# Kernel optimization log

Measured on AMD Instinct MI355X. Metric: run time of the kernel, lower is better.

The kernel has to match this reference:

```python
import jax, jax.numpy as jnp
import numpy as np

NINPUTS = 16
WIDTH = 128
KSIZE = 21
SPP = 8
BS, CI, H, W = 2, 3, 192, 192
EPS = 1e-08


def _conv(x, w, b, padding):
    y = jax.lax.conv_general_dilated(
        x, w, window_strides=(1, 1), padding=padding,
        dimension_numbers=("NCHW", "OIHW", "NCHW"))
    return y + b[None, :, None, None]


def apply_kernels(kernel, radiance, ksize):
    """Per-pixel predicted-kernel conv: fused gather-multiply-reduce over taps.
    kernel: (bs, ksize^2, kh, kw), radiance: (bs, ci, h, w).
    Replicates torch apply_kernels (normalization='sum') without materializing
    the (bs, ci, kh, kw, ksize^2) unfold tile tensor."""
    bs, k2, kh, kw = kernel.shape
    _, ci, h, w = radiance.shape
    needed = kh + ksize - 1
    if needed > h:
        crop = (needed - h) // 2
        if crop > 0:
            kernel = kernel[:, :, crop:-crop, crop:-crop]
        kh, kw = kernel.shape[2], kernel.shape[3]
    else:
        crop = (h - needed) // 2
        if crop > 0:
            radiance = radiance[:, :, crop:-crop, crop:-crop]
    taps = jnp.arange(k2, dtype=jnp.int32)
    dy = taps // ksize
    dx = taps % ksize

    def body(acc, idx):
        patch = jax.lax.dynamic_slice(radiance, (0, 0, dy[idx], dx[idx]),
                                      (bs, ci, kh, kw))
        kv = jax.lax.dynamic_slice_in_dim(kernel, idx, 1, axis=1)  # (bs,1,kh,kw)
        return acc + kv * patch, None

    acc0 = jnp.zeros((bs, ci, kh, kw), radiance.dtype)
    weighted_sum, _ = jax.lax.scan(body, acc0, taps)
    kernel_sum = jnp.sum(kernel, axis=1, keepdims=True)  # (bs,1,kh,kw)
    return weighted_sum, kernel_sum


def setup_inputs() -> dict:
    key = jax.random.key(0)
    ks = jax.random.split(key, 10)
    s = 0.05
    inp = {
        "features": jax.random.normal(ks[0], (BS, SPP, NINPUTS, H, W), jnp.float32),
        "radiance": jax.random.uniform(ks[1], (BS, SPP, CI, H, W), jnp.float32),
        # recurrent conv processor (simplified main_processor): SAME 3x3 conv
        "w_rnn": jax.random.normal(ks[2], (WIDTH, NINPUTS + WIDTH, 3, 3), jnp.float32) * s,
        "b_rnn": jnp.zeros((WIDTH,), jnp.float32),
        "w_k1": jax.random.normal(ks[3], (WIDTH, WIDTH + NINPUTS, 3, 3), jnp.float32) * s,
        "b_k1": jnp.zeros((WIDTH,), jnp.float32),
        "w_k2": jax.random.normal(ks[4], (WIDTH, WIDTH, 3, 3), jnp.float32) * s,
        "b_k2": jnp.zeros((WIDTH,), jnp.float32),
        "w_k3": jax.random.normal(ks[5], (KSIZE * KSIZE, WIDTH, 3, 3), jnp.float32) * s,
        "b_k3": jnp.zeros((KSIZE * KSIZE,), jnp.float32),
    }
    return inp


def reference(features, radiance, w_rnn, b_rnn, w_k1, b_k1, w_k2, b_k2, w_k3, b_k3):
    bs, spp, ci, h, w = radiance.shape
    lrelu = lambda x: jax.nn.leaky_relu(x, 0.01)
    state = jnp.zeros((bs, WIDTH, h, w), features.dtype)
    unnorm = sumw = max_k = None
    for step in range(spp):
        f = features[:, step]  # (bs, ninputs, h, w)
        rnn = lrelu(_conv(jnp.concatenate([f, state], axis=1), w_rnn, b_rnn, "SAME"))
        state = rnn
        nf = jnp.concatenate([rnn, f], axis=1)  # (bs, width+ninputs, h, w)
        k = lrelu(_conv(nf, w_k1, b_k1, "VALID"))
        k = lrelu(_conv(k, w_k2, b_k2, "VALID"))
        k = _conv(k, w_k3, b_k3, "VALID")  # (bs, ksize^2, h-6, w-6), linear out
        # online-softmax (flash-attention-style) running max/exp rescale
        new_max = jnp.max(k.reshape(bs, -1), axis=1).reshape(bs, 1, 1, 1)
        if step == 0:
            max_k = new_max
        else:
            old_max = max_k
            max_k = jnp.maximum(old_max, new_max)
        kern = jnp.exp(k - max_k)
        ws, ksum = apply_kernels(kern, radiance[:, step], KSIZE)
        if step == 0:
            unnorm, sumw = ws, ksum
        else:
            scale = jnp.exp(old_max - max_k)
            unnorm = unnorm * scale + ws
            sumw = sumw * scale + ksum
    return unnorm / (sumw + EPS)
```

## Files before the change

kernel.cpp:

```cpp
#include <hip/hip_runtime.h>
#include <stdint.h>

typedef _Float16 half8 __attribute__((ext_vector_type(8)));
typedef _Float16 half4 __attribute__((ext_vector_type(4)));
typedef __attribute__((ext_vector_type(8))) short short8;
typedef __attribute__((ext_vector_type(4))) float f32x4;

__device__ __forceinline__ unsigned encf(float x){
  uint32_t u = __float_as_uint(x);
  return (u & 0x80000000u) ? ~u : (u | 0x80000000u);
}
__device__ __forceinline__ float decf(unsigned u){
  uint32_t b = (u & 0x80000000u) ? (u & 0x7FFFFFFFu) : ~u;
  return __uint_as_float(b);
}
__device__ __forceinline__ void gload16(const void* g, void* l){
  __builtin_amdgcn_global_load_lds(
      (const __attribute__((address_space(1))) void*)g,
      (__attribute__((address_space(3))) void*)l, 16, 0, 0);
}

__global__ __launch_bounds__(256) void zero_u32(unsigned* __restrict__ p, int n){
  for (int i = blockIdx.x*256 + threadIdx.x; i < n; i += gridDim.x*256) p[i] = 0u;
}

__global__ __launch_bounds__(256) void pack_w(const float* __restrict__ w, _Float16* __restrict__ wp,
                                              int CO, int CI, int COP, int CINP){
  int idx = blockIdx.x*256 + threadIdx.x;
  int total = 9*COP*CINP;
  if (idx >= total) return;
  int ci = idx % CINP;
  int rest = idx / CINP;
  int co = rest % COP;
  int t  = rest / COP;
  float v = 0.f;
  if (co < CO && ci < CI) v = w[((size_t)co*CI + ci)*9 + t];
  int kc = ci >> 5, cr = ci & 31;
  wp[(((size_t)kc*9 + t)*COP + co)*32 + cr] = (_Float16)v;
}

__global__ __launch_bounds__(256) void pack_bias(const float* __restrict__ b, float* __restrict__ bp, int n, int npad){
  int i = blockIdx.x*256 + threadIdx.x;
  if (i < npad) bp[i] = (i < n) ? b[i] : 0.f;
}

__global__ __launch_bounds__(256) void pack_feat(const float* __restrict__ f,
                                                 _Float16* __restrict__ rnn_in,
                                                 _Float16* __restrict__ k1_in,
                                                 int copy_state,
                                                 unsigned fbstr, unsigned rbstr, unsigned kbstr){
  int p = blockIdx.x*256 + threadIdx.x;
  if (p >= 36864) return;
  int b = blockIdx.y;
  int y = p / 192, x = p % 192;
  const float* fb = f + (size_t)b*fbstr;
  _Float16* r = rnn_in + (size_t)b*rbstr + ((size_t)(y+1)*194 + (x+1))*160;
  _Float16* k = k1_in  + (size_t)b*kbstr + (size_t)p*160;
  #pragma unroll
  for (int c = 0; c < 16; ++c){
    _Float16 v = (_Float16)fb[c*36864 + p];
    r[c] = v;
    k[128 + c] = v;
  }
  if (copy_state){
    #pragma unroll
    for (int cc = 0; cc < 128; cc += 8)
      *reinterpret_cast<short8*>(r + 16 + cc) = *reinterpret_cast<const short8*>(k + cc);
  }
}

template<int CINP, bool RELU, bool K3>
__global__ __launch_bounds__(256, 3) void conv3(
    const _Float16* __restrict__ X, int Wst, unsigned xbstr,
    const _Float16* __restrict__ Wp, int COP,
    const float* __restrict__ bias,
    _Float16* __restrict__ Y, int Wst_out, int DCP, unsigned ybstr,
    unsigned* __restrict__ slot, int Ho, int Wo,
    int nco_mask, int nco_shift)
{
  constexpr int KC = CINP/32;
  __shared__ _Float16 lds[2][6528];

  const int tid  = threadIdx.x;
  const int lane = tid & 63;
  const int wid  = tid >> 6;
  const int wm   = wid & 1;
  const int wq   = wid >> 1;
  const int l15  = lane & 15, lg = lane >> 4;
  const int xb   = blockIdx.x * 32;
  const int yb   = blockIdx.y * 4;
  const int co_blk = blockIdx.z & nco_mask;
  const int b      = blockIdx.z >> nco_shift;
  const int co_base = co_blk * 128;

  const _Float16* Xb = X + (size_t)b * xbstr;

  uint32_t goff[4];
  #pragma unroll
  for (int k = 0; k < 4; ++k){
    int item = k*256 + tid;
    int col = item % 34;
    int q   = item / 34;
    int sg  = q & 3;
    int row = q >> 2;
    int pix = (yb + row)*Wst + xb + col;
    goff[k] = (uint32_t)(((uint32_t)pix*CINP + sg*8) * 2);
  }

  auto stage = [&](int buf, int kc){
    const char* xp = (const char*)Xb + (size_t)kc*64;
    char* lb = (char*)&lds[buf][0];
    #pragma unroll
    for (int k = 0; k < 3; ++k)
      gload16(xp + goff[k], lb + k*4096 + wid*1024);
    if (tid < 48)
      gload16(xp + goff[3], lb + 3*4096 + wid*1024);
  };

  f32x4 acc[4][4] = {};
  const _Float16* wlane = Wp + ((size_t)(co_base + wm*64 + l15)*32 + lg*8);
  const size_t wtap = (size_t)COP*32;

  stage(0, 0);
  __syncthreads();
  for (int kc = 0; kc < KC; ++kc){
    if (kc + 1 < KC) stage((kc+1)&1, kc+1);
    const _Float16* wt = wlane + (size_t)kc*9*wtap;
    const _Float16* lb = &lds[kc&1][0];
    half8 wreg[2][4];
    #pragma unroll
    for (int i = 0; i < 4; ++i)
      wreg[0][i] = *reinterpret_cast<const half8*>(wt + (size_t)i*512);
    #pragma unroll
    for (int t = 0; t < 9; ++t){
      const int cur = t & 1, nxt = cur ^ 1;
      if (t < 8){
        const _Float16* wn = wt + (size_t)(t+1)*wtap;
        #pragma unroll
        for (int i = 0; i < 4; ++i)
          wreg[nxt][i] = *reinterpret_cast<const half8*>(wn + (size_t)i*512);
      }
      const int ky = t/3, kx = t - ky*3;
      #pragma unroll
      for (int n = 0; n < 4; ++n){
        const int row = wq*2 + (n>>1) + ky;
        const int ui = ((row*4 + lg)*34 + (n&1)*16 + l15 + kx)*8;
        half8 bfrag = *reinterpret_cast<const half8*>(lb + ui);
        #pragma unroll
        for (int i = 0; i < 4; ++i)
          acc[i][n] = __builtin_amdgcn_mfma_f32_16x16x32_f16(wreg[cur][i], bfrag, acc[i][n], 0, 0, 0);
      }
    }
    if (kc + 1 < KC) __syncthreads();
  }

  float lmax = -3.0e38f;
  #pragma unroll
  for (int i = 0; i < 4; ++i){
    const int cb = co_base + wm*64 + i*16 + lg*4;
    f32x4 bs = *reinterpret_cast<const f32x4*>(bias + cb);
    #pragma unroll
    for (int n = 0; n < 4; ++n){
      const int y = yb + wq*2 + (n>>1);
      const int x = xb + (n&1)*16 + l15;
      if (y < Ho && x < Wo){
        float v[4];
        #pragma unroll
        for (int j = 0; j < 4; ++j){
          float t = acc[i][n][j] + bs[j];
          if (RELU) t = t > 0.f ? t : 0.01f*t;
          v[j] = t;
        }
        if constexpr (!K3){
          half4 pk;
          #pragma unroll
          for (int j = 0; j < 4; ++j) pk[j] = (_Float16)v[j];
          *reinterpret_cast<half4*>(Y + (size_t)b*ybstr + ((size_t)y*Wst_out + x)*DCP + cb) = pk;
        } else {
          _Float16* yp = Y + (size_t)b*ybstr;
          #pragma unroll
          for (int j = 0; j < 4; ++j){
            if (cb + j < 441){
              yp[(size_t)(cb+j)*34596 + (size_t)y*186 + x] = (_Float16)v[j];
              lmax = fmaxf(lmax, v[j]);
            }
          }
        }
      }
    }
  }
  if constexpr (K3){
    #pragma unroll
    for (int o = 32; o > 0; o >>= 1) lmax = fmaxf(lmax, __shfl_xor(lmax, o));
    if (lane == 0) atomicMax(slot + b, encf(lmax));
  }
}

__global__ void update_max(float* __restrict__ st, unsigned* __restrict__ slot, int step){
  int b = threadIdx.x;
  if (b < 2){
    float nm   = decf(slot[b]);
    float oldM = st[2*b];
    float M    = (step == 0) ? nm : fmaxf(oldM, nm);
    st[2*b+1] = (step == 0) ? 0.f : expf(oldM - M);
    st[2*b]   = M;
    slot[b] = 0u;
  }
}

__global__ __launch_bounds__(256) void apply_acc(
    const _Float16* __restrict__ k3out, const float* __restrict__ rad,
    const float* __restrict__ st,
    float* __restrict__ unnorm, float* __restrict__ sumw)
{
  const int tx = threadIdx.x & 63, ty = threadIdx.x >> 6;
  const int x = blockIdx.x*64 + tx;
  const int y = blockIdx.y*4 + ty;
  const int b = blockIdx.z;
  if (x >= 172 || y >= 172) return;
  const float M = st[2*b], scale = st[2*b+1];
  const _Float16* kp = k3out + (size_t)b*15256836 + (size_t)(y+7)*186 + (x+7);
  const float* rb = rad + (size_t)b*884736;
  float a0 = 0.f, a1 = 0.f, a2 = 0.f, aw = 0.f;
  for (int dy = 0; dy < 21; ++dy){
    const float* r0 = rb + (size_t)(y+dy)*192 + x;
    #pragma unroll
    for (int dx = 0; dx < 21; ++dx){
      float w = __expf((float)kp[(size_t)(dy*21+dx)*34596] - M);
      aw += w;
      a0 += w * r0[dx];
      a1 += w * r0[36864 + dx];
      a2 += w * r0[73728 + dx];
    }
  }
  size_t p = (size_t)b*88752 + (size_t)y*172 + x;
  size_t ps = (size_t)b*29584 + (size_t)y*172 + x;
  unnorm[p]        = unnorm[p]*scale        + a0;
  unnorm[p+29584]  = unnorm[p+29584]*scale  + a1;
  unnorm[p+59168]  = unnorm[p+59168]*scale  + a2;
  sumw[ps]         = sumw[ps]*scale         + aw;
}

__global__ __launch_bounds__(256) void finalize_out(const float* __restrict__ unnorm,
                                                    const float* __restrict__ sumw,
                                                    float* __restrict__ out){
  int i = blockIdx.x*256 + threadIdx.x;
  int b = blockIdx.y;
  if (i >= 88752) return;
  int p = i % 29584;
  out[(size_t)b*88752 + i] = unnorm[(size_t)b*88752 + i] / (sumw[(size_t)b*29584 + p] + 1e-8f);
}

extern "C" void kernel_launch(void* const* d_in, const int* in_sizes, int n_in,
                              void* d_out, int out_size, void* d_ws, size_t ws_size,
                              hipStream_t stream) {
  const float* features = (const float*)d_in[0];
  const float* radiance = (const float*)d_in[1];
  const float* w_rnn = (const float*)d_in[2];
  const float* b_rnn = (const float*)d_in[3];
  const float* w_k1  = (const float*)d_in[4];
  const float* b_k1  = (const float*)d_in[5];
  const float* w_k2  = (const float*)d_in[6];
  const float* b_k2  = (const float*)d_in[7];
  const float* w_k3  = (const float*)d_in[8];
  const float* b_k3  = (const float*)d_in[9];
  float* out = (float*)d_out;

  char* ws = (char*)d_ws;
  size_t off = 0;
  auto alloc = [&](size_t bytes)->char*{
    char* p = ws + off;
    off = (off + bytes + 255) & ~(size_t)255;
    return p;
  };
  _Float16* wp_rnn   = (_Float16*)alloc((size_t)9*128*160*2);
  _Float16* wp_k1    = (_Float16*)alloc((size_t)9*128*160*2);
  _Float16* wp_k2    = (_Float16*)alloc((size_t)9*128*128*2);
  _Float16* wp_k3    = (_Float16*)alloc((size_t)9*512*128*2);
  float*    bias_k3p = (float*)   alloc((size_t)512*4);
  const unsigned RB = 194u*194u*160u;
  const unsigned KB = (192u*192u+448u)*160u;
  const unsigned K2B = (190u*190u+444u)*128u;
  const unsigned K3B = (188u*188u+440u)*128u;
  const unsigned KOB = 441u*34596u;
  _Float16* rnn_in = (_Float16*)alloc((size_t)2*RB*2);
  _Float16* k1_in  = (_Float16*)alloc((size_t)2*KB*2);
  _Float16* k2_in  = (_Float16*)alloc((size_t)2*K2B*2);
  _Float16* k3_in  = (_Float16*)alloc((size_t)2*K3B*2);
  _Float16* k3_out = (_Float16*)alloc((size_t)2*KOB*2);
  float*    accz   = (float*)   alloc((size_t)236678*4);
  if (off > ws_size) return;

  float*    unnorm = accz;
  float*    sumw   = accz + 177504;
  float*    st     = accz + 236672;
  unsigned* slot   = (unsigned*)(accz + 236676);

  pack_w<<<(9*128*160+255)/256, 256, 0, stream>>>(w_rnn, wp_rnn, 128, 144, 128, 160);
  pack_w<<<(9*128*160+255)/256, 256, 0, stream>>>(w_k1,  wp_k1,  128, 144, 128, 160);
  pack_w<<<(9*128*128+255)/256, 256, 0, stream>>>(w_k2,  wp_k2,  128, 128, 128, 128);
  pack_w<<<(9*512*128+255)/256, 256, 0, stream>>>(w_k3,  wp_k3,  441, 128, 512, 128);
  pack_bias<<<2, 256, 0, stream>>>(b_k3, bias_k3p, 441, 512);

  zero_u32<<<2048, 256, 0, stream>>>((unsigned*)rnn_in, (int)(2*RB/2));
  zero_u32<<<925,  256, 0, stream>>>((unsigned*)accz, 236678);

  for (int s = 0; s < 8; ++s){
    const float* f   = features + (size_t)s*16*36864;
    const float* rad = radiance + (size_t)s*3*36864;
    pack_feat<<<dim3(144,2), 256, 0, stream>>>(f, rnn_in, k1_in, s > 0 ? 1 : 0,
                                               8u*16u*36864u, RB, KB);
    conv3<160,true ,false><<<dim3(6,48,2), 256, 0, stream>>>(
        rnn_in, 194, RB, wp_rnn, 128, b_rnn, k1_in, 192, 160, KB,
        nullptr, 192, 192, 0, 0);
    conv3<160,true ,false><<<dim3(6,48,2), 256, 0, stream>>>(
        k1_in, 192, KB, wp_k1, 128, b_k1, k2_in, 190, 128, K2B,
        nullptr, 190, 190, 0, 0);
    conv3<128,true ,false><<<dim3(6,47,2), 256, 0, stream>>>(
        k2_in, 190, K2B, wp_k2, 128, b_k2, k3_in, 188, 128, K3B,
        nullptr, 188, 188, 0, 0);
    conv3<128,false,true ><<<dim3(6,47,8), 256, 0, stream>>>(
        k3_in, 188, K3B, wp_k3, 512, bias_k3p, k3_out, 0, 0, KOB,
        slot, 186, 186, 3, 2);
    update_max<<<1, 64, 0, stream>>>(st, slot, s);
    apply_acc<<<dim3(3,43,2), 256, 0, stream>>>(k3_out, rad, st, unnorm, sumw);
  }
  finalize_out<<<dim3(347,2), 256, 0, stream>>>(unnorm, sumw, out);
}
```

Before: 2.739 ms.

## Switch conv3 to 32x32x16 MFMA with 16-channel K-chunks

Reworks the implicit-GEMM 3x3 conv kernel to use 32x32x16 f16 MFMA instead of 16x16x32. Weights are repacked into 32-output-channel groups with 16 input channels per chunk, and LDS staging shrinks to half-size 16-channel tiles. Each wave now owns one output row of 32 pixels and four 32-channel groups, loading a single B fragment per tap. The aim is fewer LDS reads per MFMA and less register pressure. The cost is twice as many K-chunk iterations and barriers, with smaller staged tiles.

```diff
diff --git a/kernel.cpp b/kernel.cpp
--- a/kernel.cpp
+++ b/kernel.cpp
@@ -5,6 +5,7 @@
 typedef _Float16 half4 __attribute__((ext_vector_type(4)));
 typedef __attribute__((ext_vector_type(8))) short short8;
 typedef __attribute__((ext_vector_type(4))) float f32x4;
+typedef __attribute__((ext_vector_type(16))) float f32x16;
 
 __device__ __forceinline__ unsigned encf(float x){
   uint32_t u = __float_as_uint(x);
@@ -35,8 +36,8 @@
   int t  = rest / COP;
   float v = 0.f;
   if (co < CO && ci < CI) v = w[((size_t)co*CI + ci)*9 + t];
-  int kc = ci >> 5, cr = ci & 31;
-  wp[(((size_t)kc*9 + t)*COP + co)*32 + cr] = (_Float16)v;
+  int kc = ci >> 4, chl = ci & 15;
+  wp[(((size_t)kc*9 + t)*(COP/32) + (co>>5))*512 + (co&31)*16 + chl] = (_Float16)v;
 }
 
 __global__ __launch_bounds__(256) void pack_bias(const float* __restrict__ b, float* __restrict__ bp, int n, int npad){
@@ -78,15 +79,14 @@
     unsigned* __restrict__ slot, int Ho, int Wo,
     int nco_mask, int nco_shift)
 {
-  constexpr int KC = CINP/32;
-  __shared__ _Float16 lds[2][6528];
+  constexpr int KC = CINP/16;
+  __shared__ _Float16 lds[2][3264];
 
   const int tid  = threadIdx.x;
   const int lane = tid & 63;
   const int wid  = tid >> 6;
-  const int wm   = wid & 1;
-  const int wq   = wid >> 1;
-  const int l15  = lane & 15, lg = lane >> 4;
+  const int l31  = lane & 31;
+  const int hsel = lane >> 5;
   const int xb   = blockIdx.x * 32;
   const int yb   = blockIdx.y * 4;
   const int co_blk = blockIdx.z & nco_mask;
@@ -95,81 +95,79 @@
 
   const _Float16* Xb = X + (size_t)b * xbstr;
 
-  uint32_t goff[4];
+  uint32_t goff[2];
   #pragma unroll
-  for (int k = 0; k < 4; ++k){
+  for (int k = 0; k < 2; ++k){
     int item = k*256 + tid;
-    int col = item % 34;
-    int q   = item / 34;
-    int sg  = q & 3;
-    int row = q >> 2;
-    int pix = (yb + row)*Wst + xb + col;
-    goff[k] = (uint32_t)(((uint32_t)pix*CINP + sg*8) * 2);
+    if (item < 408){
+      int row  = item / 68;
+      int rem  = item % 68;
+      int col  = rem >> 1;
+      int half = rem & 1;
+      int pix  = (yb + row)*Wst + xb + col;
+      goff[k] = (uint32_t)(((uint32_t)pix*CINP + half*8) * 2);
+    } else goff[k] = 0;
   }
 
   auto stage = [&](int buf, int kc){
-    const char* xp = (const char*)Xb + (size_t)kc*64;
+    const char* xp = (const char*)Xb + (size_t)kc*32;
     char* lb = (char*)&lds[buf][0];
-    #pragma unroll
-    for (int k = 0; k < 3; ++k)
-      gload16(xp + goff[k], lb + k*4096 + wid*1024);
-    if (tid < 48)
-      gload16(xp + goff[3], lb + 3*4096 + wid*1024);
+    gload16(xp + goff[0], lb + wid*1024);
+    if (tid < 152)
+      gload16(xp + goff[1], lb + 4096 + wid*1024);
   };
 
-  f32x4 acc[4][4] = {};
-  const _Float16* wlane = Wp + ((size_t)(co_base + wm*64 + l15)*32 + lg*8);
-  const size_t wtap = (size_t)COP*32;
+  const uint32_t blane = (uint32_t)(l31*16 + hsel*8);
+
+  f32x16 acc[4] = {};
+  const _Float16* wlane = Wp + ((size_t)co_blk*4)*512 + l31*16 + hsel*8;
+  const int NG = COP/32;
 
   stage(0, 0);
   __syncthreads();
   for (int kc = 0; kc < KC; ++kc){
     if (kc + 1 < KC) stage((kc+1)&1, kc+1);
-    const _Float16* wt = wlane + (size_t)kc*9*wtap;
+    const _Float16* wt = wlane + (size_t)(kc*9)*NG*512;
     const _Float16* lb = &lds[kc&1][0];
-    half8 wreg[2][4];
-    #pragma unroll
-    for (int i = 0; i < 4; ++i)
-      wreg[0][i] = *reinterpret_cast<const half8*>(wt + (size_t)i*512);
+    half8 wreg[2][4], breg[2];
+    #pragma unroll
+    for (int g = 0; g < 4; ++g)
+      wreg[0][g] = *reinterpret_cast<const half8*>(wt + g*512);
+    breg[0] = *reinterpret_cast<const half8*>(lb + (wid*34)*16 + blane);
     #pragma unroll
     for (int t = 0; t < 9; ++t){
       const int cur = t & 1, nxt = cur ^ 1;
       if (t < 8){
-        const _Float16* wn = wt + (size_t)(t+1)*wtap;
+        const int ky = (t+1)/3, kx = (t+1) - ky*3;
+        const _Float16* wn = wt + (size_t)(t+1)*NG*512;
         #pragma unroll
-        for (int i = 0; i < 4; ++i)
-          wreg[nxt][i] = *reinterpret_cast<const half8*>(wn + (size_t)i*512);
+        for (int g = 0; g < 4; ++g)
+          wreg[nxt][g] = *reinterpret_cast<const half8*>(wn + g*512);
+        breg[nxt] = *reinterpret_cast<const half8*>(lb + (((wid+ky)*34) + kx)*16 + blane);
       }
-      const int ky = t/3, kx = t - ky*3;
       #pragma unroll
-      for (int n = 0; n < 4; ++n){
-        const int row = wq*2 + (n>>1) + ky;
-        const int ui = ((row*4 + lg)*34 + (n&1)*16 + l15 + kx)*8;
-        half8 bfrag = *reinterpret_cast<const half8*>(lb + ui);
-        #pragma unroll
-        for (int i = 0; i < 4; ++i)
-          acc[i][n] = __builtin_amdgcn_mfma_f32_16x16x32_f16(wreg[cur][i], bfrag, acc[i][n], 0, 0, 0);
-      }
+      for (int g = 0; g < 4; ++g)
+        acc[g] = __builtin_amdgcn_mfma_f32_32x32x16_f16(wreg[cur][g], breg[cur], acc[g], 0, 0, 0);
     }
     if (kc + 1 < KC) __syncthreads();
   }
 
+  const int y = yb + wid;
+  const int x = xb + l31;
   float lmax = -3.0e38f;
-  #pragma unroll
-  for (int i = 0; i < 4; ++i){
-    const int cb = co_base + wm*64 + i*16 + lg*4;
-    f32x4 bs = *reinterpret_cast<const f32x4*>(bias + cb);
-    #pragma unroll
-    for (int n = 0; n < 4; ++n){
-      const int y = yb + wq*2 + (n>>1);
-      const int x = xb + (n&1)*16 + l15;
-      if (y < Ho && x < Wo){
+  if (y < Ho && x < Wo){
+    #pragma unroll
+    for (int g = 0; g < 4; ++g){
+      #pragma unroll
+      for (int q = 0; q < 4; ++q){
+        const int cb = co_base + g*32 + 4*hsel + 8*q;
+        f32x4 bs = *reinterpret_cast<const f32x4*>(bias + cb);
         float v[4];
         #pragma unroll
         for (int j = 0; j < 4; ++j){
-          float t = acc[i][n][j] + bs[j];
-          if (RELU) t = t > 0.f ? t : 0.01f*t;
-          v[j] = t;
+          float tv = acc[g][q*4 + j] + bs[j];
+          if (RELU) tv = tv > 0.f ? tv : 0.01f*tv;
+          v[j] = tv;
         }
         if constexpr (!K3){
           half4 pk;
```

Result: slower. 3.450 ms (+25.9%).
